# Kernel optimization log

Hardware: AMD Instinct MI355X
Metric: run time of the kernel (lower is better)

Reference implementation:

```python
import jax, jax.numpy as jnp
import numpy as np

DROP_PROB = 0.1
BLOCK_SIZE = 7  # odd -> no even-size trim branch
N, C, H, W = 64, 256, 28, 28


def conv3x3(x, w):
    # x: [N,C,H,W], w: [O,I,3,3], stride 1, SAME padding
    return jax.lax.conv_general_dilated(
        x, w, window_strides=(1, 1), padding='SAME',
        dimension_numbers=('NCHW', 'OIHW', 'NCHW'))


def setup_inputs() -> dict:
    key = jax.random.key(0)
    k1, k2, k3, k4 = jax.random.split(key, 4)
    x = jax.random.normal(k1, (N, C, H, W), jnp.float32)
    # learned conv weights for the two branches (layer3 and premodel.layer3)
    w_layer3 = jax.random.normal(k2, (C, C, 3, 3), jnp.float32) * 0.05
    w_pre = jax.random.normal(k3, (C, C, 3, 3), jnp.float32) * 0.05
    # uniform draws used for the Bernoulli(gamma) drop mask, shape (N,H,W)
    mask_u = jax.random.uniform(k4, (N, H, W), jnp.float32)
    return {'x': x, 'w_layer3': w_layer3, 'w_pre': w_pre, 'mask_u': mask_u}


def reference(x, w_layer3, w_pre, mask_u):
    gamma = DROP_PROB / (BLOCK_SIZE ** 2)
    a = conv3x3(x, w_layer3)   # x = self.layer3(x)
    b = conv3x3(x, w_pre)      # output4 = self.premodel.layer3(x)
    # mask = (rand(N,H,W) < gamma).float()
    mask = (mask_u < gamma).astype(x.dtype)  # [N,H,W]
    # block_mask = 1 - max_pool2d(mask, k=block_size, stride=1, pad=block_size//2)
    pooled = jax.lax.reduce_window(
        mask, -jnp.inf, jax.lax.max,
        window_dimensions=(1, BLOCK_SIZE, BLOCK_SIZE),
        window_strides=(1, 1, 1), padding='SAME')
    block_mask = 1.0 - pooled  # [N,H,W]
    # fused blend: keep layer3 output where block_mask==1, else premodel output
    out = jnp.where(block_mask[:, None, :, :] == 1.0, a, b)  # [N,C,H,W]
    # out * block_mask.numel() / block_mask.sum()
    scale = jnp.asarray(block_mask.size, x.dtype) / jnp.sum(block_mask)
    return out * scale
```

## Files before the change

### kernel.cpp

```cpp
#include <hip/hip_runtime.h>
#include <hip/hip_bf16.h>


typedef __bf16  bf16x8 __attribute__((ext_vector_type(8)));
typedef float   f32x4  __attribute__((ext_vector_type(4)));
typedef short   short8 __attribute__((ext_vector_type(8)));
typedef unsigned int u32;
typedef unsigned short u16;

#define XT_OFF     65536
#define WT_OFF     29556736
#define LISTA_OFF  31916032
#define LISTB_OFF  32116736
#define SLOT       22528

__device__ __forceinline__ u16 f2bf(float v) {
    u32 u = __float_as_uint(v);
    u32 r = (u + 0x7FFFu + ((u >> 16) & 1u)) >> 16;
    return (u16)r;
}

__device__ __forceinline__ void gll16(const void* g, void* l) {
    __builtin_amdgcn_global_load_lds(
        (const __attribute__((address_space(1))) u32*)g,
        (__attribute__((address_space(3))) u32*)l, 16, 0, 0);
}

__global__ __launch_bounds__(256)
void prep_xt(const float* __restrict__ x, u16* __restrict__ xt) {
    __shared__ u16 sm[64 * 790];
    const int n = blockIdx.x >> 2, ct = blockIdx.x & 3;
    const int tid = threadIdx.x;
    u32* b32 = (u32*)(xt + (size_t)n * 230400);

    if (ct == 0) {
        #pragma unroll
        for (int i = 0; i < 15; ++i) {
            int k = i * 256 + tid;
            b32[k] = 0;
            b32[111360 + k] = 0;
        }
        #pragma unroll
        for (int i = 0; i < 14; ++i) {
            int k = i * 256 + tid;
            int oh = 1 + (k >> 7), c2 = k & 127;
            b32[(oh * 30) * 128 + c2] = 0;
            b32[(oh * 30 + 29) * 128 + c2] = 0;
        }
    }

    const float4* s4 = (const float4*)(x + (size_t)n * 200704) + ct * 12544;
    char* smb = (char*)sm;
    #pragma unroll 7
    for (int i = 0; i < 49; ++i) {
        int q = i * 256 + tid;
        float4 v = s4[q];
        int lc = q / 196, r = q % 196;
        u32* dst = (u32*)(smb + lc * 1580 + r * 8);
        dst[0] = (u32)f2bf(v.x) | ((u32)f2bf(v.y) << 16);
        dst[1] = (u32)f2bf(v.z) | ((u32)f2bf(v.w) << 16);
    }
    __syncthreads();

    const int cpp = tid & 31, sl = tid >> 5;
    const char* srow0 = smb + (2 * cpp) * 1580;
    const char* srow1 = srow0 + 1580;
    #pragma unroll 7
    for (int t2 = 0; t2 < 98; ++t2) {
        int hw = sl * 98 + t2;
        int h = hw / 28, w = hw % 28;
        u32 v = (u32)*(const u16*)(srow0 + hw * 2)
              | ((u32)*(const u16*)(srow1 + hw * 2) << 16);
        b32[((1 + h) * 30 + 1 + w) * 128 + ct * 32 + cpp] = v;
    }
}

__global__ __launch_bounds__(256)
void prep_rest(const float* __restrict__ wl,
               const float* __restrict__ wp,
               const float* __restrict__ mu,
               u16* __restrict__ wt,
               int* __restrict__ listA, int* __restrict__ listB,
               int* __restrict__ cntB, int* __restrict__ cntA) {
    int b = blockIdx.x, tid = threadIdx.x;
    if (b < 576) {
        int gid = b * 256 + tid;
        int base = gid << 3;
        int bb = base >> 12;
        int e = base & 4095;
        int t = bb >> 2, nq = bb & 3;
        int kk = t >> 3;
        int row = e >> 5, ps = (e & 31) >> 3;
        int c0 = (t & 7) * 32 + ((ps ^ ((row >> 1) & 3)) << 3);
        int o = nq * 128 + row;
        const float* wsrc = (o < 256) ? wl : wp;
        const float* wr = wsrc + ((size_t)(o & 255) * 256 + c0) * 9 + kk;
        short8 v;
        #pragma unroll
        for (int j = 0; j < 8; ++j) v[j] = (short)f2bf(wr[j * 9]);
        *(short8*)(wt + base) = v;
    } else {
        __shared__ float uf[784];
        __shared__ int cnts[2][16];
        __shared__ int bases[2];
        const int n = b - 576;
        const float* un = mu + n * 784;
        for (int i = tid; i < 784; i += 256) uf[i] = un[i];
        __syncthreads();
        const float g = (float)(0.1 / 49.0);
        const int wid = tid >> 6, ln = tid & 63;
        unsigned long long balB[4], balA[4];
        int pbit[4];
        #pragma unroll
        for (int it = 0; it < 4; ++it) {
            int i = it * 256 + tid;
            int a = (i < 784);
            int p = 0;
            if (a) {
                int h = i / 28, w = i % 28;
                for (int dy = -3; dy <= 3; ++dy) {
                    int hh = h + dy;
                    if (hh < 0 || hh >= 28) continue;
                    for (int dx = -3; dx <= 3; ++dx) {
                        int ww = w + dx;
                        if (ww < 0 || ww >= 28) continue;
                        p |= (uf[hh * 28 + ww] < g) ? 1 : 0;
                    }
                }
            }
            pbit[it] = p;
            balB[it] = __ballot(a && p);
            balA[it] = __ballot(a != 0);
            if (ln == 0) {
                int c1 = __popcll(balB[it]);
                cnts[1][it * 4 + wid] = c1;
                cnts[0][it * 4 + wid] = __popcll(balA[it]) - c1;
            }
        }
        __syncthreads();
        if (tid == 0) {
            int tB = 0, tA = 0;
            #pragma unroll
            for (int s = 0; s < 16; ++s) { tB += cnts[1][s]; tA += cnts[0][s]; }
            bases[1] = atomicAdd(cntB, tB);
            bases[0] = atomicAdd(cntA, tA);
        }
        __syncthreads();
        #pragma unroll
        for (int it = 0; it < 4; ++it) {
            int i = it * 256 + tid;
            if (i >= 784) continue;
            int slot = it * 4 + wid;
            int offB = 0, offA = 0;
            for (int s = 0; s < slot; ++s) { offB += cnts[1][s]; offA += cnts[0][s]; }
            unsigned long long below = (1ULL << ln) - 1;
            int r1 = __popcll(balB[it] & below);
            int rA = __popcll(balA[it] & below) - r1;
            int m = n * 784 + i;
            if (pbit[it]) listB[bases[1] + offB + r1] = m;
            else          listA[bases[0] + offA + rA] = m;
        }
    }
}

__global__ __launch_bounds__(256, 2)
void conv_kernel(const char* __restrict__ xt,
                 const char* __restrict__ wt,
                 const int* __restrict__ listA,
                 const int* __restrict__ listB,
                 const int* __restrict__ dropped,
                 float* __restrict__ out) {
    __shared__ char smem[55296];
    const int tid = threadIdx.x;
    const int lb = (blockIdx.x & 7) * 57 + (blockIdx.x >> 3);
    const int vt = lb >> 1;
    const int nh = lb & 1;
    const int cB = *dropped;
    const int cA = 50176 - cB;
    const int naT = (cA + 223) / 224;
    const int nbT = (cB + 223) / 224;
    if (vt >= naT + nbT) return;
    const int branch = (vt >= naT) ? 1 : 0;
    const int tix = branch ? (vt - naT) : vt;
    const int cnt = branch ? cB : cA;
    const int* lst = branch ? listB : listA;
    const int nq = branch * 2 + nh;
    const int lane = tid & 63, wave = tid >> 6;
    const int lane15 = lane & 15, grp = lane >> 4;
    const int wm = wave >> 1, wn = wave & 1;

    long pbA[4];
    {
        int swz = ((tid & 3) ^ ((tid >> 3) & 3)) << 4;
        #pragma unroll
        for (int i = 0; i < 4; ++i) {
            int r = i * 64 + (tid >> 2);
            int idx = tix * 224 + r;
            if (idx >= cnt) idx = cnt - 1;
            int m = lst[idx];
            int n = m / 784, rem = m % 784;
            pbA[i] = (long)(((n * 30 + rem / 28 + 1) * 30 + (rem % 28 + 1)) * 512
                            + swz);
        }
    }

    f32x4 acc[7][4];
    #pragma unroll
    for (int i = 0; i < 7; ++i)
        #pragma unroll
        for (int j = 0; j < 4; ++j)
            acc[i][j] = (f32x4){0.f, 0.f, 0.f, 0.f};

    const int so  = (grp ^ ((lane15 >> 1) & 3)) << 4;
    const int arb = wm * 7168 + (lane15 << 6) + so;
    const int brb = 14336 + wn * 4096 + (lane15 << 6) + so;

#define AON(TC) ((long)((TC) >> 3) / 3 * 15360 + (long)(((TC) >> 3) % 3) * 512 \
                 - 15872 + (long)(((TC) & 7) << 6))
#define STG(TC, SL) { char* sd_ = smem + (SL) * SLOT;                       \
        const long ao_ = AON(TC);                                           \
        gll16(xt + pbA[0] + ao_, sd_ + (tid << 4));                         \
        gll16(xt + pbA[1] + ao_, sd_ + 4096 + (tid << 4));                  \
        gll16(xt + pbA[2] + ao_, sd_ + 8192 + (tid << 4));                  \
        if (tid < 128) gll16(xt + pbA[3] + ao_, sd_ + 12288 + (tid << 4));  \
        const char* wb_ = wt + ((size_t)((TC) * 4 + nq) << 13);             \
        gll16(wb_ + (tid << 4), sd_ + 14336 + (tid << 4));                  \
        gll16(wb_ + 4096 + (tid << 4), sd_ + 18432 + (tid << 4)); }
#define DS_AV0(dst, SL) { const char* sb_ = smem + (SL) * SLOT;             \
        _Pragma("unroll")                                                   \
        for (int fm = 0; fm < 4; ++fm)                                      \
            dst[fm] = *(const bf16x8*)(sb_ + arb + (fm << 10)); }
#define DS_AV1(dst, SL) { const char* sb_ = smem + (SL) * SLOT + 4096;      \
        _Pragma("unroll")                                                   \
        for (int fm = 0; fm < 3; ++fm)                                      \
            dst[fm] = *(const bf16x8*)(sb_ + arb + (fm << 10)); }
#define DS_BV(dst, SL) { const char* sb_ = smem + (SL) * SLOT;              \
        _Pragma("unroll")                                                   \
        for (int fn = 0; fn < 4; ++fn)                                      \
            dst[fn] = *(const bf16x8*)(sb_ + brb + (fn << 10)); }
#define MM(A0_, NF, AV, BV) { __builtin_amdgcn_s_setprio(1);                \
        _Pragma("unroll")                                                   \
        for (int fm = 0; fm < (NF); ++fm)                                   \
            _Pragma("unroll")                                               \
            for (int fn = 0; fn < 4; ++fn)                                  \
                acc[(A0_)+fm][fn] = __builtin_amdgcn_mfma_f32_16x16x32_bf16( \
                    AV[fm], BV[fn], acc[(A0_)+fm][fn], 0, 0, 0);            \
        __builtin_amdgcn_s_setprio(0); }
#define LGKM(N) { asm volatile("s_waitcnt lgkmcnt(" #N ")" ::: "memory");   \
                  __builtin_amdgcn_sched_barrier(0); }
#define VM0     { asm volatile("s_waitcnt vmcnt(0)" ::: "memory");          \
                  __builtin_amdgcn_sched_barrier(0); }
#define BAR     asm volatile("s_barrier" ::: "memory")

    bf16x8 av0[4], av1[3], bv[4];

    STG(0, 0);
    VM0;
    BAR;

    for (int t = 0; t < 72; ++t) {
        const int sc = t & 1, ss = sc ^ 1;
        if (t < 71) STG(t + 1, ss);
        DS_AV0(av0, sc);
        DS_BV(bv, sc);
        DS_AV1(av1, sc);
        LGKM(3);
        MM(0, 4, av0, bv);
        LGKM(0);
        MM(4, 3, av1, bv);
        VM0;
        BAR;
    }

    float scale = 50176.0f / (float)(50176 - cB);
    float* ep = (float*)smem + wave * 2080;
    __syncthreads();
    #pragma unroll
    for (int rr = 0; rr < 4; ++rr) {
        const int r2 = rr & 1;
        const int mh = rr >> 1;
        const int nf = mh ? 3 : 4;
        for (int fm2 = 0; fm2 < nf; ++fm2)
            #pragma unroll
            for (int f2 = 0; f2 < 2; ++f2)
                #pragma unroll
                for (int j = 0; j < 4; ++j)
                    ep[(f2 * 16 + lane15) * 65 + fm2 * 16 + grp * 4 + j] =
                        acc[mh * 4 + fm2][r2 * 2 + f2][j];
        __syncthreads();
        {
            int gidx = tix * 224 + wm * 112 + mh * 64 + lane;
            if ((mh == 0 || lane < 48) && gidx < cnt) {
                int m = lst[gidx];
                int n = m / 784, rem = m % 784;
                size_t ob = (size_t)n * 200704 + rem;
                #pragma unroll
                for (int ch = 0; ch < 32; ++ch) {
                    int c = nh * 128 + wn * 64 + r2 * 32 + ch;
                    out[ob + (size_t)c * 784] = ep[ch * 65 + lane] * scale;
                }
            }
        }
        __syncthreads();
    }
#undef AON
#undef STG
#undef DS_AV0
#undef DS_AV1
#undef DS_BV
#undef MM
#undef LGKM
#undef VM0
#undef BAR
}

extern "C" void kernel_launch(void* const* d_in, const int* in_sizes, int n_in,
                              void* d_out, int out_size, void* d_ws, size_t ws_size,
                              hipStream_t stream) {
    const float* x  = (const float*)d_in[0];
    const float* wl = (const float*)d_in[1];
    const float* wp = (const float*)d_in[2];
    const float* mu = (const float*)d_in[3];
    float* out = (float*)d_out;
    char* ws = (char*)d_ws;

    int* cntB = (int*)ws;
    int* cntA = (int*)(ws + 4);
    u16* xt = (u16*)(ws + XT_OFF);
    u16* wt = (u16*)(ws + WT_OFF);
    int* listA = (int*)(ws + LISTA_OFF);
    int* listB = (int*)(ws + LISTB_OFF);

    hipMemsetAsync(ws, 0, 8, stream);

    prep_xt<<<256, 256, 0, stream>>>(x, xt);
    prep_rest<<<640, 256, 0, stream>>>(wl, wp, mu, wt, listA, listB, cntB, cntA);
    conv_kernel<<<456, 256, 0, stream>>>((const char*)xt, (const char*)wt,
                                         listA, listB, cntB, out);
}
```

Baseline: 104.8 us.

## Widen conv tiles to full 256 output channels with 4-stage LDS pipeline

Each conv block now covers all 256 output channels of one branch using 512 threads and 8 waves, instead of splitting channels across two blocks. This halves redundant staging of the activation tile. The weight layout is rearranged to match. The main loop becomes a 4-slot prefetch ring with loads issued three tiles ahead, partial vmcnt waits, and A/B fragment double-buffering, so global loads overlap MFMA work. LDS per block grows to 120KB, which lowers occupancy and reduces the number of blocks to 232.

```diff
diff --git a/kernel.cpp b/kernel.cpp
--- a/kernel.cpp
+++ b/kernel.cpp
@@ -12,7 +12,7 @@
 #define WT_OFF     29556736
 #define LISTA_OFF  31916032
 #define LISTB_OFF  32116736
-#define SLOT       22528
+#define SLOT       30720
 
 __device__ __forceinline__ u16 f2bf(float v) {
     u32 u = __float_as_uint(v);
@@ -86,15 +86,14 @@
     if (b < 576) {
         int gid = b * 256 + tid;
         int base = gid << 3;
-        int bb = base >> 12;
-        int e = base & 4095;
-        int t = bb >> 2, nq = bb & 3;
+        int bb = base >> 13;
+        int e = base & 8191;
+        int t = bb >> 1, bn = bb & 1;
         int kk = t >> 3;
         int row = e >> 5, ps = (e & 31) >> 3;
         int c0 = (t & 7) * 32 + ((ps ^ ((row >> 1) & 3)) << 3);
-        int o = nq * 128 + row;
-        const float* wsrc = (o < 256) ? wl : wp;
-        const float* wr = wsrc + ((size_t)(o & 255) * 256 + c0) * 9 + kk;
+        const float* wsrc = bn ? wp : wl;
+        const float* wr = wsrc + ((size_t)row * 256 + c0) * 9 + kk;
         short8 v;
         #pragma unroll
         for (int j = 0; j < 8; ++j) v[j] = (short)f2bf(wr[j * 9]);
@@ -163,45 +162,43 @@
     }
 }
 
-__global__ __launch_bounds__(256, 2)
+__global__ __launch_bounds__(512, 2)
 void conv_kernel(const char* __restrict__ xt,
                  const char* __restrict__ wt,
                  const int* __restrict__ listA,
                  const int* __restrict__ listB,
                  const int* __restrict__ dropped,
                  float* __restrict__ out) {
-    __shared__ char smem[55296];
+    __shared__ char smem[122880];
     const int tid = threadIdx.x;
-    const int lb = (blockIdx.x & 7) * 57 + (blockIdx.x >> 3);
-    const int vt = lb >> 1;
-    const int nh = lb & 1;
+    const int lb = (blockIdx.x & 7) * 29 + (blockIdx.x >> 3);
     const int cB = *dropped;
     const int cA = 50176 - cB;
     const int naT = (cA + 223) / 224;
     const int nbT = (cB + 223) / 224;
-    if (vt >= naT + nbT) return;
-    const int branch = (vt >= naT) ? 1 : 0;
-    const int tix = branch ? (vt - naT) : vt;
+    if (lb >= naT + nbT) return;
+    const int branch = (lb >= naT) ? 1 : 0;
+    const int tix = branch ? (lb - naT) : lb;
     const int cnt = branch ? cB : cA;
     const int* lst = branch ? listB : listA;
-    const int nq = branch * 2 + nh;
     const int lane = tid & 63, wave = tid >> 6;
     const int lane15 = lane & 15, grp = lane >> 4;
-    const int wm = wave >> 1, wn = wave & 1;
-
-    long pbA[4];
+    const int wm = wave >> 2, wn = wave & 3;
+
+    long pb0, pb1;
     {
+        int i = tid >> 2;
         int swz = ((tid & 3) ^ ((tid >> 3) & 3)) << 4;
-        #pragma unroll
-        for (int i = 0; i < 4; ++i) {
-            int r = i * 64 + (tid >> 2);
-            int idx = tix * 224 + r;
-            if (idx >= cnt) idx = cnt - 1;
-            int m = lst[idx];
-            int n = m / 784, rem = m % 784;
-            pbA[i] = (long)(((n * 30 + rem / 28 + 1) * 30 + (rem % 28 + 1)) * 512
-                            + swz);
-        }
+        int i0 = tix * 224 + i;
+        if (i0 >= cnt) i0 = cnt - 1;
+        int m0 = lst[i0];
+        int n0 = m0 / 784, re0 = m0 % 784;
+        pb0 = (long)(((n0 * 30 + re0 / 28 + 1) * 30 + (re0 % 28 + 1)) * 512 + swz);
+        int i1 = tix * 224 + 96 + i;
+        if (i1 >= cnt) i1 = cnt - 1;
+        int m1 = lst[i1];
+        int n1 = m1 / 784, re1 = m1 % 784;
+        pb1 = (long)(((n1 * 30 + re1 / 28 + 1) * 30 + (re1 % 28 + 1)) * 512 + swz);
     }
 
     f32x4 acc[7][4];
@@ -217,15 +214,6 @@
 
 #define AON(TC) ((long)((TC) >> 3) / 3 * 15360 + (long)(((TC) >> 3) % 3) * 512 \
                  - 15872 + (long)(((TC) & 7) << 6))
-#define STG(TC, SL) { char* sd_ = smem + (SL) * SLOT;                       \
-        const long ao_ = AON(TC);                                           \
-        gll16(xt + pbA[0] + ao_, sd_ + (tid << 4));                         \
-        gll16(xt + pbA[1] + ao_, sd_ + 4096 + (tid << 4));                  \
-        gll16(xt + pbA[2] + ao_, sd_ + 8192 + (tid << 4));                  \
-        if (tid < 128) gll16(xt + pbA[3] + ao_, sd_ + 12288 + (tid << 4));  \
-        const char* wb_ = wt + ((size_t)((TC) * 4 + nq) << 13);             \
-        gll16(wb_ + (tid << 4), sd_ + 14336 + (tid << 4));                  \
-        gll16(wb_ + 4096 + (tid << 4), sd_ + 18432 + (tid << 4)); }
 #define DS_AV0(dst, SL) { const char* sb_ = smem + (SL) * SLOT;             \
         _Pragma("unroll")                                                   \
         for (int fm = 0; fm < 4; ++fm)                                      \
@@ -238,6 +226,14 @@
         _Pragma("unroll")                                                   \
         for (int fn = 0; fn < 4; ++fn)                                      \
             dst[fn] = *(const bf16x8*)(sb_ + brb + (fn << 10)); }
+#define STG_A(TC, SL) { char* sd_ = smem + (SL) * SLOT;                     \
+        const long ao_ = AON(TC);                                           \
+        gll16(xt + pb0 + ao_, sd_ + (tid << 4));                            \
+        gll16(xt + pb1 + ao_, sd_ + 6144 + (tid << 4)); }
+#define STG_B(TC, SL) { char* sd_ = smem + (SL) * SLOT + 14336;             \
+        const char* wb_ = wt + ((size_t)((TC) * 2 + branch) << 14);         \
+        gll16(wb_ + (tid << 4), sd_ + (tid << 4));                          \
+        gll16(wb_ + 8192 + (tid << 4), sd_ + 8192 + (tid << 4)); }
 #define MM(A0_, NF, AV, BV) { __builtin_amdgcn_s_setprio(1);                \
         _Pragma("unroll")                                                   \
         for (int fm = 0; fm < (NF); ++fm)                                   \
@@ -248,28 +244,75 @@
         __builtin_amdgcn_s_setprio(0); }
 #define LGKM(N) { asm volatile("s_waitcnt lgkmcnt(" #N ")" ::: "memory");   \
                   __builtin_amdgcn_sched_barrier(0); }
-#define VM0     { asm volatile("s_waitcnt vmcnt(0)" ::: "memory");          \
+#define VM(N)   { asm volatile("s_waitcnt vmcnt(" #N ")" ::: "memory");     \
                   __builtin_amdgcn_sched_barrier(0); }
 #define BAR     asm volatile("s_barrier" ::: "memory")
 
-    bf16x8 av0[4], av1[3], bv[4];
-
-    STG(0, 0);
-    VM0;
+    bf16x8 av0[4], av1[3], bv0[4], bv1[4];
+
+    #pragma unroll
+    for (int tt = 0; tt < 3; ++tt) {
+        STG_A(tt, tt);
+        STG_B(tt, tt);
+    }
+    VM(8);
     BAR;
-
-    for (int t = 0; t < 72; ++t) {
-        const int sc = t & 1, ss = sc ^ 1;
-        if (t < 71) STG(t + 1, ss);
-        DS_AV0(av0, sc);
-        DS_BV(bv, sc);
-        DS_AV1(av1, sc);
+    DS_AV0(av0, 0);
+    DS_BV(bv0, 0);
+
+    for (int u = 0; u < 35; ++u) {
+        const int te = 2 * u, to = te + 1;
+        {
+            const int sc = te & 3, sn = to & 3, ss = (te + 3) & 3;
+            int tc = te + 3; if (tc > 71) tc = 71;
+            DS_AV1(av1, sc);
+            STG_A(tc, ss);
+            LGKM(3);
+            MM(0, 4, av0, bv0);
+            VM(6);
+            BAR;
+            DS_AV0(av0, sn);
+            DS_BV(bv1, sn);
+            STG_B(tc, ss);
+            LGKM(8);
+            MM(4, 3, av1, bv0);
+            BAR;
+        }
+        {
+            const int sc = to & 3, sn = (to + 1) & 3, ss = (to + 3) & 3;
+            int tc = to + 3; if (tc > 71) tc = 71;
+            DS_AV1(av1, sc);
+            STG_A(tc, ss);
+            LGKM(3);
+            MM(0, 4, av0, bv1);
+            VM(6);
+            BAR;
+            DS_AV0(av0, sn);
+            DS_BV(bv0, sn);
+            STG_B(tc, ss);
+            LGKM(8);
+            MM(4, 3, av1, bv1);
+            BAR;
+        }
+    }
+    {
+        DS_AV1(av1, 2);
+        STG_A(71, 1);
         LGKM(3);
-        MM(0, 4, av0, bv);
+        MM(0, 4, av0, bv0);
+        VM(6);
+        BAR;
+        DS_AV0(av0, 3);
+        DS_BV(bv1, 3);
+        STG_B(71, 1);
+        LGKM(8);
+        MM(4, 3, av1, bv0);
+        BAR;
+        DS_AV1(av1, 3);
+        LGKM(3);
+        MM(0, 4, av0, bv1);
         LGKM(0);
-        MM(4, 3, av1, bv);
-        VM0;
-        BAR;
+        MM(4, 3, av1, bv1);
     }
 
     float scale = 50176.0f / (float)(50176 - cB);
@@ -296,7 +339,7 @@
                 size_t ob = (size_t)n * 200704 + rem;
                 #pragma unroll
                 for (int ch = 0; ch < 32; ++ch) {
-                    int c = nh * 128 + wn * 64 + r2 * 32 + ch;
+                    int c = wn * 64 + r2 * 32 + ch;
                     out[ob + (size_t)c * 784] = ep[ch * 65 + lane] * scale;
                 }
             }
@@ -304,13 +347,14 @@
         __syncthreads();
     }
 #undef AON
-#undef STG
 #undef DS_AV0
 #undef DS_AV1
 #undef DS_BV
+#undef STG_A
+#undef STG_B
 #undef MM
 #undef LGKM
-#undef VM0
+#undef VM
 #undef BAR
 }
 
@@ -335,6 +379,6 @@
 
     prep_xt<<<256, 256, 0, stream>>>(x, xt);
     prep_rest<<<640, 256, 0, stream>>>(wl, wp, mu, wt, listA, listB, cntB, cntA);
-    conv_kernel<<<456, 256, 0, stream>>>((const char*)xt, (const char*)wt,
+    conv_kernel<<<232, 512, 0, stream>>>((const char*)xt, (const char*)wt,
                                          listA, listB, cntB, out);
 }
```

New measurement: 105.4 us. Within noise of the previous version (+0.5%).
